# Kernel tuning notes

Measured on AMD Instinct MI355X. Metric: run time of the kernel, lower is better.

Reference implementation:

```python
import jax, jax.numpy as jnp
import numpy as np

B, S, D, H, L = 32, 512, 1024, 1024, 2
SCALE = 1.0 / np.sqrt(H)  # keep activations sane


def setup_inputs() -> dict:
    key = jax.random.key(0)
    ks = jax.random.split(key, 9)
    return {
        "x":   jax.random.normal(ks[0], (B, S, D), dtype=jnp.float32),
        "Wx0": jax.random.normal(ks[1], (4 * H, D), dtype=jnp.float32) * SCALE,
        "Wh0": jax.random.normal(ks[2], (4 * H, H), dtype=jnp.float32) * SCALE,
        "bx0": jax.random.normal(ks[3], (4 * H,), dtype=jnp.float32) * SCALE,
        "bh0": jax.random.normal(ks[4], (4 * H,), dtype=jnp.float32) * SCALE,
        "Wx1": jax.random.normal(ks[5], (4 * H, H), dtype=jnp.float32) * SCALE,
        "Wh1": jax.random.normal(ks[6], (4 * H, H), dtype=jnp.float32) * SCALE,
        "bx1": jax.random.normal(ks[7], (4 * H,), dtype=jnp.float32) * SCALE,
        "bh1": jax.random.normal(ks[8], (4 * H,), dtype=jnp.float32) * SCALE,
    }


def reference(x, Wx0, Wh0, bx0, bh0, Wx1, Wh1, bx1, bh1):
    Wx, Wh, bx, bh = [Wx0, Wx1], [Wh0, Wh1], [bx0, bx1], [bh0, bh1]

    def step(carry, x_t):
        h, c = carry                      # each [L, B, H]
        inp = x_t                         # [B, D]
        hs, cs = [], []
        for l in range(L):
            gates = inp @ Wx[l].T + bx[l] + h[l] @ Wh[l].T + bh[l]  # [B, 4H]
            f, i, g, o = jnp.split(gates, 4, axis=1)  # torch chunk order: f,i,g,o
            c_new = jax.nn.sigmoid(f) * c[l] + jax.nn.sigmoid(i) * jnp.tanh(g)
            h_new = jax.nn.sigmoid(o) * jnp.tanh(c_new)  # proj is Identity
            hs.append(h_new)
            cs.append(c_new)
            inp = h_new  # dropout p=0 -> identity
        return (jnp.stack(hs), jnp.stack(cs)), hs[-1]

    h0 = jnp.zeros((L, B, H), dtype=x.dtype)
    c0 = jnp.zeros((L, B, H), dtype=x.dtype)
    (h_n, c_n), outs = jax.lax.scan(step, (h0, c0), jnp.transpose(x, (1, 0, 2)))
    outputs = jnp.transpose(outs, (1, 0, 2))  # [B, S, H] (batch_first)
    return outputs, (h_n, c_n)
```

## Files before the change

kernel.cpp:

```cpp
#include <hip/hip_runtime.h>
#include <math.h>

#define Bsz 32
#define Ssz 512
#define Hsz 1024

typedef _Float16 f16x8 __attribute__((ext_vector_type(8)));
typedef float    f32x4 __attribute__((ext_vector_type(4)));
typedef float    f32x8 __attribute__((ext_vector_type(8)));
typedef unsigned u32x4 __attribute__((ext_vector_type(4)));

struct P {
  const float *x, *Wx0, *Wh0, *bx0, *bh0, *Wx1, *Wh1, *bx1, *bh1;
  unsigned *h0r;
  unsigned *h1r;
  unsigned *cnt0, *cnt1;
  _Float16 *wsw;
  float *out;
};

__global__ __launch_bounds__(256) void preconv(P p) {
  unsigned idx   = blockIdx.x * 256 + threadIdx.x;
  unsigned lane  = idx & 63;
  unsigned m     = (idx >> 6) & 3;
  unsigned ks    = (idx >> 8) & 63;
  unsigned blk   = (idx >> 14) & 63;
  unsigned layer = idx >> 20;
  unsigned hidx  = blk * 16 + (lane & 15);
  unsigned k     = ks * 32 + (lane >> 4) * 8;
  unsigned row   = m * 1024 + hidx;
  const float* src;
  if (layer == 0) src = (k < 1024) ? p.Wx0 + (size_t)row * 1024 + k
                                   : p.Wh0 + (size_t)row * 1024 + (k - 1024);
  else            src = (k < 1024) ? p.Wx1 + (size_t)row * 1024 + k
                                   : p.Wh1 + (size_t)row * 1024 + (k - 1024);
  f32x8 v = *reinterpret_cast<const f32x8*>(src);
  f16x8 h;
#pragma unroll
  for (int j = 0; j < 8; ++j) h[j] = (_Float16)v[j];
  *reinterpret_cast<f16x8*>(p.wsw + (size_t)idx * 8) = h;
}

__device__ inline void load_bfrag(const unsigned* rowp, f16x8& Bh, f16x8& Bl) {
  u32x4 hw, lw;
  const unsigned long long* q = (const unsigned long long*)rowp;
#pragma unroll
  for (int j = 0; j < 4; ++j) {
    unsigned long long u = __hip_atomic_load(q + j, __ATOMIC_RELAXED, __HIP_MEMORY_SCOPE_AGENT);
    unsigned a = (unsigned)u, b = (unsigned)(u >> 32);
    hw[j] = (a & 0xffffu) | (b << 16);
    lw[j] = (a >> 16) | (b & 0xffff0000u);
  }
  Bh = __builtin_bit_cast(f16x8, hw);
  Bl = __builtin_bit_cast(f16x8, lw);
}

__device__ inline void load_xfrag(const float* xp, f16x8& Bh, f16x8& Bl) {
  f32x8 v = *reinterpret_cast<const f32x8*>(xp);
#pragma unroll
  for (int j = 0; j < 8; ++j) {
    _Float16 hv = (_Float16)v[j];
    Bh[j] = hv; Bl[j] = (_Float16)(v[j] - (float)hv);
  }
}

__global__ __launch_bounds__(512, 2) void lstm_persist(P p) {
  const int blk   = blockIdx.x;
  const int layer = blk >> 6;
  const int hb    = blk & 63;
  const int tid   = threadIdx.x;
  const int w     = tid >> 6;
  const int lane  = tid & 63;
  const int nl    = lane & 15;
  const int quad  = lane >> 4;

  __shared__ float red[8][64 * 33];
  __shared__ float csl[Bsz * 16];
  __shared__ float bsum[64];

  if (tid < 64) {
    int r = (tid >> 4) * 1024 + hb * 16 + (tid & 15);
    bsum[tid] = layer ? (p.bx1[r] + p.bh1[r]) : (p.bx0[r] + p.bh0[r]);
  }
  csl[tid] = 0.f;
  __syncthreads();

  const _Float16* wslab = p.wsw + (size_t)(layer * 64 + hb) * 131072;
  f16x8 Wr[32];
#pragma unroll
  for (int kk = 0; kk < 8; ++kk)
#pragma unroll
    for (int m = 0; m < 4; ++m)
      Wr[kk * 4 + m] = *reinterpret_cast<const f16x8*>(
          wslab + (size_t)(((w * 8 + kk) * 4 + m) * 64 + lane) * 8);

  const bool xwave = (layer == 0) && (w < 4);
  const int  kloc  = (w & 3) * 256;

  for (int s = 0; s < Ssz; ++s) {
    if (tid == 0) {
      if (layer == 0) {
        if (s > 0)
          while (__hip_atomic_load(p.cnt0 + (s - 1), __ATOMIC_RELAXED, __HIP_MEMORY_SCOPE_AGENT) < 64u) {}
        if (s >= 4)
          while (__hip_atomic_load(p.cnt1 + (s - 4), __ATOMIC_RELAXED, __HIP_MEMORY_SCOPE_AGENT) < 64u) {}
      } else {
        while (__hip_atomic_load(p.cnt0 + s, __ATOMIC_RELAXED, __HIP_MEMORY_SCOPE_AGENT) < 64u) {}
        if (s > 0)
          while (__hip_atomic_load(p.cnt1 + (s - 1), __ATOMIC_RELAXED, __HIP_MEMORY_SCOPE_AGENT) < 64u) {}
      }
    }
    __syncthreads();

    const unsigned* bring = nullptr;
    if (layer == 0) { if (!xwave) bring = p.h0r + ((s - 1) & 3) * 32768 + kloc; }
    else {
      if (w < 4) bring = p.h0r + (s & 3) * 32768 + kloc;
      else       bring = p.h1r + ((s - 1) & 1) * 32768 + kloc;
    }
    const float* xbase = p.x + (size_t)s * 1024 + kloc;

    f32x4 acc[4][2];
#pragma unroll
    for (int m = 0; m < 4; ++m)
#pragma unroll
      for (int nt = 0; nt < 2; ++nt) acc[m][nt] = (f32x4){0.f, 0.f, 0.f, 0.f};

    f16x8 Bh[2][2], Bl[2][2];
    if (xwave) {
      load_xfrag(xbase + (size_t)nl        * (Ssz * 1024) + quad * 8, Bh[0][0], Bl[0][0]);
      load_xfrag(xbase + (size_t)(nl + 16) * (Ssz * 1024) + quad * 8, Bh[0][1], Bl[0][1]);
    } else {
      load_bfrag(bring + nl * 1024        + quad * 8, Bh[0][0], Bl[0][0]);
      load_bfrag(bring + (nl + 16) * 1024 + quad * 8, Bh[0][1], Bl[0][1]);
    }
#pragma unroll
    for (int kk = 0; kk < 8; ++kk) {
      const int cur = kk & 1, nxt = cur ^ 1;
      if (kk < 7) {
        const int ko = (kk + 1) * 32 + quad * 8;
        if (xwave) {
          load_xfrag(xbase + (size_t)nl        * (Ssz * 1024) + ko, Bh[nxt][0], Bl[nxt][0]);
          load_xfrag(xbase + (size_t)(nl + 16) * (Ssz * 1024) + ko, Bh[nxt][1], Bl[nxt][1]);
        } else {
          load_bfrag(bring + nl * 1024        + ko, Bh[nxt][0], Bl[nxt][0]);
          load_bfrag(bring + (nl + 16) * 1024 + ko, Bh[nxt][1], Bl[nxt][1]);
        }
      }
#pragma unroll
      for (int m = 0; m < 4; ++m) {
        f16x8 A = Wr[kk * 4 + m];
#pragma unroll
        for (int nt = 0; nt < 2; ++nt) {
          acc[m][nt] = __builtin_amdgcn_mfma_f32_16x16x32_f16(A, Bh[cur][nt], acc[m][nt], 0, 0, 0);
          acc[m][nt] = __builtin_amdgcn_mfma_f32_16x16x32_f16(A, Bl[cur][nt], acc[m][nt], 0, 0, 0);
        }
      }
    }

#pragma unroll
    for (int m = 0; m < 4; ++m)
#pragma unroll
      for (int nt = 0; nt < 2; ++nt)
#pragma unroll
        for (int r = 0; r < 4; ++r)
          red[w][(m * 16 + quad * 4 + r) * 33 + nt * 16 + nl] = acc[m][nt][r];
    __syncthreads();
#pragma unroll
    for (int j = 0; j < 4; ++j) {
      int idx = tid + j * 512;
      int ad = (idx >> 5) * 33 + (idx & 31);
      float ssum = red[0][ad] + red[1][ad] + red[2][ad] + red[3][ad]
                 + red[4][ad] + red[5][ad] + red[6][ad] + red[7][ad];
      red[0][ad] = ssum;
    }
    __syncthreads();

    {
      int hl = tid & 15, b = tid >> 4;
      float gf = red[0][(0 * 16 + hl) * 33 + b] + bsum[0 * 16 + hl];
      float gi = red[0][(1 * 16 + hl) * 33 + b] + bsum[1 * 16 + hl];
      float gg = red[0][(2 * 16 + hl) * 33 + b] + bsum[2 * 16 + hl];
      float go = red[0][(3 * 16 + hl) * 33 + b] + bsum[3 * 16 + hl];
      float f  = 1.f / (1.f + __expf(-gf));
      float i  = 1.f / (1.f + __expf(-gi));
      float g  = tanhf(gg);
      float o  = 1.f / (1.f + __expf(-go));
      float c  = f * csl[b * 16 + hl] + i * g;
      float hn = o * tanhf(c);
      csl[b * 16 + hl] = c;
      _Float16 hh  = (_Float16)hn;
      _Float16 hlo = (_Float16)(hn - (float)hh);
      unsigned pk = (unsigned)__builtin_bit_cast(unsigned short, hh)
                  | ((unsigned)__builtin_bit_cast(unsigned short, hlo) << 16);
      int hg = hb * 16 + hl;
      if (layer == 0) {
        __hip_atomic_store(p.h0r + (s & 3) * 32768 + b * 1024 + hg, pk,
                           __ATOMIC_RELAXED, __HIP_MEMORY_SCOPE_AGENT);
      } else {
        __hip_atomic_store(p.h1r + (s & 1) * 32768 + b * 1024 + hg, pk,
                           __ATOMIC_RELAXED, __HIP_MEMORY_SCOPE_AGENT);
        p.out[(size_t)b * (Ssz * Hsz) + (size_t)s * Hsz + hg] = hn;
      }
      if (s == Ssz - 1) {
        float* tail = p.out + (size_t)Bsz * Ssz * Hsz;
        tail[layer * 32768 + b * 1024 + hg] = hn;
        tail[65536 + layer * 32768 + b * 1024 + hg] = c;
      }
    }
    __syncthreads();
    if (tid == 0)
      __hip_atomic_fetch_add((layer ? p.cnt1 : p.cnt0) + s, 1u,
                             __ATOMIC_RELAXED, __HIP_MEMORY_SCOPE_AGENT);
  }
}

extern "C" void kernel_launch(void* const* d_in, const int* in_sizes, int n_in,
                              void* d_out, int out_size, void* d_ws, size_t ws_size,
                              hipStream_t stream) {
  char* ws = (char*)d_ws;
  P p;
  p.x   = (const float*)d_in[0];
  p.Wx0 = (const float*)d_in[1]; p.Wh0 = (const float*)d_in[2];
  p.bx0 = (const float*)d_in[3]; p.bh0 = (const float*)d_in[4];
  p.Wx1 = (const float*)d_in[5]; p.Wh1 = (const float*)d_in[6];
  p.bx1 = (const float*)d_in[7]; p.bh1 = (const float*)d_in[8];

  p.h0r  = (unsigned*)(ws);
  p.h1r  = (unsigned*)(ws + 524288);
  p.cnt0 = (unsigned*)(ws + 786432);
  p.cnt1 = (unsigned*)(ws + 788480);
  p.wsw  = (_Float16*)(ws + 1048576);
  p.out  = (float*)d_out;

  hipMemsetAsync(d_ws, 0, 1048576, stream);
  preconv<<<dim3(8192), dim3(256), 0, stream>>>(p);
  lstm_persist<<<dim3(128), dim3(512), 0, stream>>>(p);
}
```

Before: 8.692 ms.

## Replace block-wide step counters with per-block flags polled per wave

Replaces the per-step global counters (one thread spins, then a block barrier) with per-producer-block step flags kept in small ring buffers. Each wave spins only on the flags of the 16 producer blocks whose hidden slice it reads, so waves can start their matmul independently and the pre-step __syncthreads is removed. The recurrent-state loads are also restructured into a triple-buffered batch of raw atomic loads issued ahead of the unpack and MFMA work, to hide load latency. This adds more polling traffic from 64 lanes per wave and relies on relaxed atomics for ordering, plus extra register pressure from the load buffers.

```diff
diff --git a/kernel.cpp b/kernel.cpp
--- a/kernel.cpp
+++ b/kernel.cpp
@@ -14,7 +14,7 @@
   const float *x, *Wx0, *Wh0, *bx0, *bh0, *Wx1, *Wh1, *bx1, *bh1;
   unsigned *h0r;
   unsigned *h1r;
-  unsigned *cnt0, *cnt1;
+  unsigned *f0, *f1;
   _Float16 *wsw;
   float *out;
 };
@@ -41,20 +41,6 @@
   *reinterpret_cast<f16x8*>(p.wsw + (size_t)idx * 8) = h;
 }
 
-__device__ inline void load_bfrag(const unsigned* rowp, f16x8& Bh, f16x8& Bl) {
-  u32x4 hw, lw;
-  const unsigned long long* q = (const unsigned long long*)rowp;
-#pragma unroll
-  for (int j = 0; j < 4; ++j) {
-    unsigned long long u = __hip_atomic_load(q + j, __ATOMIC_RELAXED, __HIP_MEMORY_SCOPE_AGENT);
-    unsigned a = (unsigned)u, b = (unsigned)(u >> 32);
-    hw[j] = (a & 0xffffu) | (b << 16);
-    lw[j] = (a >> 16) | (b & 0xffff0000u);
-  }
-  Bh = __builtin_bit_cast(f16x8, hw);
-  Bl = __builtin_bit_cast(f16x8, lw);
-}
-
 __device__ inline void load_xfrag(const float* xp, f16x8& Bh, f16x8& Bl) {
   f32x8 v = *reinterpret_cast<const f32x8*>(xp);
 #pragma unroll
@@ -98,27 +84,29 @@
   const int  kloc  = (w & 3) * 256;
 
   for (int s = 0; s < Ssz; ++s) {
-    if (tid == 0) {
-      if (layer == 0) {
-        if (s > 0)
-          while (__hip_atomic_load(p.cnt0 + (s - 1), __ATOMIC_RELAXED, __HIP_MEMORY_SCOPE_AGENT) < 64u) {}
-        if (s >= 4)
-          while (__hip_atomic_load(p.cnt1 + (s - 4), __ATOMIC_RELAXED, __HIP_MEMORY_SCOPE_AGENT) < 64u) {}
-      } else {
-        while (__hip_atomic_load(p.cnt0 + s, __ATOMIC_RELAXED, __HIP_MEMORY_SCOPE_AGENT) < 64u) {}
-        if (s > 0)
-          while (__hip_atomic_load(p.cnt1 + (s - 1), __ATOMIC_RELAXED, __HIP_MEMORY_SCOPE_AGENT) < 64u) {}
-      }
-    }
-    __syncthreads();
-
-    const unsigned* bring = nullptr;
-    if (layer == 0) { if (!xwave) bring = p.h0r + ((s - 1) & 3) * 32768 + kloc; }
-    else {
-      if (w < 4) bring = p.h0r + (s & 3) * 32768 + kloc;
-      else       bring = p.h1r + ((s - 1) & 1) * 32768 + kloc;
-    }
-    const float* xbase = p.x + (size_t)s * 1024 + kloc;
+    if (layer == 0) {
+      if (xwave) {
+        if (s >= 4) {
+          const unsigned* fp = p.f1 + (s & 1) * 64 + lane;
+          unsigned need = (unsigned)(s - 3);
+          while (__hip_atomic_load(fp, __ATOMIC_RELAXED, __HIP_MEMORY_SCOPE_AGENT) < need) {}
+        }
+      } else if (s >= 1) {
+        const unsigned* fp = p.f0 + ((s - 1) & 3) * 64 + (w & 3) * 16 + nl;
+        unsigned need = (unsigned)s;
+        while (__hip_atomic_load(fp, __ATOMIC_RELAXED, __HIP_MEMORY_SCOPE_AGENT) < need) {}
+      }
+    } else {
+      if (w < 4) {
+        const unsigned* fp = p.f0 + (s & 3) * 64 + (w & 3) * 16 + nl;
+        unsigned need = (unsigned)(s + 1);
+        while (__hip_atomic_load(fp, __ATOMIC_RELAXED, __HIP_MEMORY_SCOPE_AGENT) < need) {}
+      } else if (s >= 1) {
+        const unsigned* fp = p.f1 + ((s - 1) & 1) * 64 + (w & 3) * 16 + nl;
+        unsigned need = (unsigned)s;
+        while (__hip_atomic_load(fp, __ATOMIC_RELAXED, __HIP_MEMORY_SCOPE_AGENT) < need) {}
+      }
+    }
 
     f32x4 acc[4][2];
 #pragma unroll
@@ -126,36 +114,83 @@
 #pragma unroll
       for (int nt = 0; nt < 2; ++nt) acc[m][nt] = (f32x4){0.f, 0.f, 0.f, 0.f};
 
-    f16x8 Bh[2][2], Bl[2][2];
     if (xwave) {
+      const float* xbase = p.x + (size_t)s * 1024 + kloc;
+      f16x8 Bh[2][2], Bl[2][2];
       load_xfrag(xbase + (size_t)nl        * (Ssz * 1024) + quad * 8, Bh[0][0], Bl[0][0]);
       load_xfrag(xbase + (size_t)(nl + 16) * (Ssz * 1024) + quad * 8, Bh[0][1], Bl[0][1]);
-    } else {
-      load_bfrag(bring + nl * 1024        + quad * 8, Bh[0][0], Bl[0][0]);
-      load_bfrag(bring + (nl + 16) * 1024 + quad * 8, Bh[0][1], Bl[0][1]);
-    }
-#pragma unroll
-    for (int kk = 0; kk < 8; ++kk) {
-      const int cur = kk & 1, nxt = cur ^ 1;
-      if (kk < 7) {
-        const int ko = (kk + 1) * 32 + quad * 8;
-        if (xwave) {
+#pragma unroll
+      for (int kk = 0; kk < 8; ++kk) {
+        const int cur = kk & 1, nxt = cur ^ 1;
+        if (kk < 7) {
+          const int ko = (kk + 1) * 32 + quad * 8;
           load_xfrag(xbase + (size_t)nl        * (Ssz * 1024) + ko, Bh[nxt][0], Bl[nxt][0]);
           load_xfrag(xbase + (size_t)(nl + 16) * (Ssz * 1024) + ko, Bh[nxt][1], Bl[nxt][1]);
-        } else {
-          load_bfrag(bring + nl * 1024        + ko, Bh[nxt][0], Bl[nxt][0]);
-          load_bfrag(bring + (nl + 16) * 1024 + ko, Bh[nxt][1], Bl[nxt][1]);
-        }
-      }
-#pragma unroll
-      for (int m = 0; m < 4; ++m) {
-        f16x8 A = Wr[kk * 4 + m];
-#pragma unroll
-        for (int nt = 0; nt < 2; ++nt) {
-          acc[m][nt] = __builtin_amdgcn_mfma_f32_16x16x32_f16(A, Bh[cur][nt], acc[m][nt], 0, 0, 0);
-          acc[m][nt] = __builtin_amdgcn_mfma_f32_16x16x32_f16(A, Bl[cur][nt], acc[m][nt], 0, 0, 0);
-        }
-      }
+        }
+#pragma unroll
+        for (int m = 0; m < 4; ++m) {
+          f16x8 A = Wr[kk * 4 + m];
+#pragma unroll
+          for (int nt = 0; nt < 2; ++nt) {
+            acc[m][nt] = __builtin_amdgcn_mfma_f32_16x16x32_f16(A, Bh[cur][nt], acc[m][nt], 0, 0, 0);
+            acc[m][nt] = __builtin_amdgcn_mfma_f32_16x16x32_f16(A, Bl[cur][nt], acc[m][nt], 0, 0, 0);
+          }
+        }
+      }
+    } else {
+      const unsigned* bring;
+      if (layer == 0) bring = p.h0r + ((s - 1) & 3) * 32768 + kloc;
+      else if (w < 4) bring = p.h0r + (s & 3) * 32768 + kloc;
+      else            bring = p.h1r + ((s - 1) & 1) * 32768 + kloc;
+      const unsigned long long* q0 =
+          (const unsigned long long*)(bring + nl * 1024) + quad * 4;
+      const unsigned long long* q1 =
+          (const unsigned long long*)(bring + (nl + 16) * 1024) + quad * 4;
+
+      unsigned long long raw[3][8];
+#define ISSUE(KK) do {                                                            \
+      const unsigned long long* r0_ = q0 + (KK) * 16;                             \
+      const unsigned long long* r1_ = q1 + (KK) * 16;                             \
+      _Pragma("unroll")                                                           \
+      for (int j_ = 0; j_ < 4; ++j_) {                                            \
+        raw[(KK) % 3][j_]     = __hip_atomic_load(r0_ + j_, __ATOMIC_RELAXED,     \
+                                                  __HIP_MEMORY_SCOPE_AGENT);      \
+        raw[(KK) % 3][4 + j_] = __hip_atomic_load(r1_ + j_, __ATOMIC_RELAXED,     \
+                                                  __HIP_MEMORY_SCOPE_AGENT);      \
+      }                                                                           \
+    } while (0)
+#define UNPACK(BUF, OFF, BH, BL) do {                                             \
+      u32x4 hw_, lw_;                                                             \
+      _Pragma("unroll")                                                           \
+      for (int j_ = 0; j_ < 4; ++j_) {                                            \
+        unsigned long long u_ = raw[BUF][(OFF) + j_];                             \
+        unsigned a_ = (unsigned)u_, b_ = (unsigned)(u_ >> 32);                    \
+        hw_[j_] = (a_ & 0xffffu) | (b_ << 16);                                    \
+        lw_[j_] = (a_ >> 16) | (b_ & 0xffff0000u);                                \
+      }                                                                           \
+      BH = __builtin_bit_cast(f16x8, hw_);                                        \
+      BL = __builtin_bit_cast(f16x8, lw_);                                        \
+    } while (0)
+
+      ISSUE(0); ISSUE(1); ISSUE(2);
+#pragma unroll
+      for (int kk = 0; kk < 8; ++kk) {
+        const int buf = kk % 3;
+        f16x8 Bh0, Bl0, Bh1, Bl1;
+        UNPACK(buf, 0, Bh0, Bl0);
+        UNPACK(buf, 4, Bh1, Bl1);
+        if (kk < 5) ISSUE(kk + 3);
+#pragma unroll
+        for (int m = 0; m < 4; ++m) {
+          f16x8 A = Wr[kk * 4 + m];
+          acc[m][0] = __builtin_amdgcn_mfma_f32_16x16x32_f16(A, Bh0, acc[m][0], 0, 0, 0);
+          acc[m][0] = __builtin_amdgcn_mfma_f32_16x16x32_f16(A, Bl0, acc[m][0], 0, 0, 0);
+          acc[m][1] = __builtin_amdgcn_mfma_f32_16x16x32_f16(A, Bh1, acc[m][1], 0, 0, 0);
+          acc[m][1] = __builtin_amdgcn_mfma_f32_16x16x32_f16(A, Bl1, acc[m][1], 0, 0, 0);
+        }
+      }
+#undef ISSUE
+#undef UNPACK
     }
 
 #pragma unroll
@@ -209,9 +244,14 @@
       }
     }
     __syncthreads();
-    if (tid == 0)
-      __hip_atomic_fetch_add((layer ? p.cnt1 : p.cnt0) + s, 1u,
-                             __ATOMIC_RELAXED, __HIP_MEMORY_SCOPE_AGENT);
+    if (tid == 0) {
+      if (layer == 0)
+        __hip_atomic_store(p.f0 + (s & 3) * 64 + hb, (unsigned)(s + 1),
+                           __ATOMIC_RELAXED, __HIP_MEMORY_SCOPE_AGENT);
+      else
+        __hip_atomic_store(p.f1 + (s & 1) * 64 + hb, (unsigned)(s + 1),
+                           __ATOMIC_RELAXED, __HIP_MEMORY_SCOPE_AGENT);
+    }
   }
 }
 
@@ -226,12 +266,12 @@
   p.Wx1 = (const float*)d_in[5]; p.Wh1 = (const float*)d_in[6];
   p.bx1 = (const float*)d_in[7]; p.bh1 = (const float*)d_in[8];
 
-  p.h0r  = (unsigned*)(ws);
-  p.h1r  = (unsigned*)(ws + 524288);
-  p.cnt0 = (unsigned*)(ws + 786432);
-  p.cnt1 = (unsigned*)(ws + 788480);
-  p.wsw  = (_Float16*)(ws + 1048576);
-  p.out  = (float*)d_out;
+  p.h0r = (unsigned*)(ws);
+  p.h1r = (unsigned*)(ws + 524288);
+  p.f0  = (unsigned*)(ws + 786432);
+  p.f1  = (unsigned*)(ws + 788480);
+  p.wsw = (_Float16*)(ws + 1048576);
+  p.out = (float*)d_out;
 
   hipMemsetAsync(d_ws, 0, 1048576, stream);
   preconv<<<dim3(8192), dim3(256), 0, stream>>>(p);
```

New measurement: 8.924 ms. +2.7%, slower.
